# Performance work log

Hardware: AMD Instinct MI355X
Metric: run time of the kernel (lower is better)

The kernel has to match this reference:

```python
import jax, jax.numpy as jnp
import numpy as np

BUCKET_BINS = jnp.array([0, 1, 2, 3, 4, 5, 7, 8, 9, 10, 15, 16, 31, 32, 63, 64], dtype=jnp.int64)
POS_NUM = 28  # ZHPosTaging.pos_num; table size pos_num + 1


def setup_inputs() -> dict:
    key = jax.random.key(0)
    k1, k2, k3, k4, k5 = jax.random.split(key, 5)
    B, S, D = 4, 2048, 768
    N = 4096
    W, P = 20, 20
    x = jax.random.normal(k1, (B, S, D), dtype=jnp.float32)
    spans = jnp.sort(jax.random.randint(k2, (N, 2), 0, S, dtype=jnp.int64), axis=-1)
    pt_labels = jax.random.randint(k3, (S,), 0, POS_NUM + 1, dtype=jnp.int64)
    width_table = jax.random.normal(k4, (16, W), dtype=jnp.float32)
    pos_table = jax.random.normal(k5, (POS_NUM + 1, P), dtype=jnp.float32)
    return {"x": x, "spans": spans, "pt_labels": pt_labels,
            "width_table": width_table, "pos_table": pos_table}


def reference(x, spans, pt_labels, width_table, pos_table):
    # x: [B,S,D], spans: [N,2] with s0<=s1, pt_labels: [S]
    s0, s1 = spans[:, 0], spans[:, 1]                      # [N]
    width = s1 - s0 + 1                                    # [N], >= 1
    # bucket index: last ix with width >= BUCKET_BINS[ix]
    em = jnp.searchsorted(BUCKET_BINS, width, side='right') - 1
    width_emb = width_table[em]                            # [N,W]
    pos_emb0 = pos_table[pt_labels[s0]]                    # [N,P]
    pos_emb1 = pos_table[pt_labels[s1]]                    # [N,P]
    # segment mean over x[:, s0:s1+1] via exclusive cumsum
    cs = jnp.concatenate([jnp.zeros_like(x[:, :1]), jnp.cumsum(x, axis=1)], axis=1)  # [B,S+1,D]
    span_sum = cs[:, s1 + 1] - cs[:, s0]                   # [B,N,D]
    mean_vec = span_sum / width[None, :, None].astype(x.dtype)
    xs0 = x[:, s0]                                         # [B,N,D]
    xs1 = x[:, s1]                                         # [B,N,D]
    B, N = x.shape[0], spans.shape[0]
    bcast = lambda e: jnp.broadcast_to(e[None], (B, N, e.shape[-1]))
    return jnp.concatenate(
        [mean_vec, xs0, bcast(pos_emb0), xs1, bcast(pos_emb1), bcast(width_emb)],
        axis=-1)                                           # [B,N,3D+2P+W]
```

## Files before the change

kernel.cpp:

```cpp
#include <hip/hip_runtime.h>

#define BB   4
#define SS   2048
#define DD   768
#define NN   4096
#define PW   20
#define CH   16
#define NCH  128
#define ROW  2364

typedef float f4 __attribute__((ext_vector_type(4)));

__global__ __launch_bounds__(256) void partial_kernel(const float* __restrict__ x,
                                                      float* __restrict__ partial) {
    int d = blockIdx.x * 256 + threadIdx.x;
    int c = blockIdx.y;
    int b = blockIdx.z;
    const float* xp = x + ((size_t)(b * SS + c * CH)) * DD + d;
    float s = 0.f;
#pragma unroll
    for (int i = 0; i < CH; ++i) s += xp[(size_t)i * DD];
    partial[(b * NCH + c) * DD + d] = s;
}

__global__ __launch_bounds__(256) void prefix_kernel(float* __restrict__ partial) {
    int t = blockIdx.x * 256 + threadIdx.x;
    int b = t / DD;
    int d = t - b * DD;
    float* p = partial + (size_t)b * NCH * DD + d;
    float v[NCH];
#pragma unroll
    for (int c = 0; c < NCH; ++c) v[c] = p[(size_t)c * DD];
    float run = 0.f;
#pragma unroll
    for (int c = 0; c < NCH; ++c) { float nv = run + v[c]; p[(size_t)c * DD] = run; run = nv; }
}

__global__ __launch_bounds__(256) void cumsum_kernel(const float* __restrict__ x,
                                                     const float* __restrict__ partial,
                                                     float* __restrict__ cs) {
    int d = blockIdx.x * 256 + threadIdx.x;
    int c = blockIdx.y;
    int b = blockIdx.z;
    float run = partial[(b * NCH + c) * DD + d];
    const float* xp = x + ((size_t)(b * SS) + c * CH) * DD + d;
    float*       cp = cs + ((size_t)(b * (SS + 1)) + c * CH + 1) * DD + d;
    if (c == 0) cs[((size_t)(b * (SS + 1))) * DD + d] = 0.f;
    float v[CH];
#pragma unroll
    for (int i = 0; i < CH; ++i) v[i] = xp[(size_t)i * DD];
#pragma unroll
    for (int i = 0; i < CH; ++i) { run += v[i]; cp[(size_t)i * DD] = run; }
}

__global__ __launch_bounds__(192) void gather_kernel(const float* __restrict__ x,
                                                     const int* __restrict__ spans,
                                                     const int* __restrict__ pt_labels,
                                                     const float* __restrict__ wtab,
                                                     const float* __restrict__ ptab,
                                                     const float* __restrict__ cs,
                                                     float* __restrict__ out) {
    int n = blockIdx.x;
    int b = blockIdx.y;
    int t = threadIdx.x;

    int s0 = spans[2 * n];
    int s1 = spans[2 * n + 1];
    int width = s1 - s0 + 1;
    float inv_w = 1.0f / (float)width;

    const int bins[15] = {1, 2, 3, 4, 5, 7, 8, 9, 10, 15, 16, 31, 32, 63, 64};
    int em = 0;
#pragma unroll
    for (int i = 0; i < 15; ++i) em += (width >= bins[i]) ? 1 : 0;

    const f4* cs0 = (const f4*)(cs + ((size_t)(b * (SS + 1)) + s0) * DD);
    const f4* cs1 = (const f4*)(cs + ((size_t)(b * (SS + 1)) + s1 + 1) * DD);
    const f4* x0  = (const f4*)(x + ((size_t)(b * SS) + s0) * DD);
    const f4* x1  = (const f4*)(x + ((size_t)(b * SS) + s1) * DD);
    f4* o = (f4*)(out + ((size_t)(b * NN) + n) * ROW);

    f4 a  = cs0 == cs1 ? cs1[t] : cs1[t];
    f4 c0 = cs0[t];
    f4 v0 = x0[t];
    f4 v1 = x1[t];
    f4 m = (a - c0) * inv_w;
    __builtin_nontemporal_store(m,  o + t);
    __builtin_nontemporal_store(v0, o + 192 + t);
    __builtin_nontemporal_store(v1, o + 389 + t);

    if (t < 15) {
        int l0 = pt_labels[s0];
        int l1 = pt_labels[s1];
        if (t < 5) {
            f4 e = ((const f4*)(ptab + l0 * PW))[t];
            __builtin_nontemporal_store(e, o + 384 + t);
        } else if (t < 10) {
            f4 e = ((const f4*)(ptab + l1 * PW))[t - 5];
            __builtin_nontemporal_store(e, o + 581 + (t - 5));
        } else {
            f4 e = ((const f4*)(wtab + em * PW))[t - 10];
            __builtin_nontemporal_store(e, o + 586 + (t - 10));
        }
    }
}

extern "C" void kernel_launch(void* const* d_in, const int* in_sizes, int n_in,
                              void* d_out, int out_size, void* d_ws, size_t ws_size,
                              hipStream_t stream) {
    const float* x     = (const float*)d_in[0];
    const int*   spans = (const int*)d_in[1];
    const int*   pt    = (const int*)d_in[2];
    const float* wtab  = (const float*)d_in[3];
    const float* ptab  = (const float*)d_in[4];
    float* out = (float*)d_out;

    float* cs      = (float*)d_ws;
    float* partial = cs + (size_t)BB * (SS + 1) * DD;

    dim3 g1(3, NCH, BB);
    partial_kernel<<<g1, 256, 0, stream>>>(x, partial);
    prefix_kernel<<<12, 256, 0, stream>>>(partial);
    cumsum_kernel<<<g1, 256, 0, stream>>>(x, partial, cs);
    gather_kernel<<<dim3(NN, BB), 192, 0, stream>>>(x, spans, pt, wtab, ptab, cs, out);
}
```

Before: 213.6 us.

## Vectorize cumsum kernels with float4 and fold batch loop into gather blocks

```diff
diff --git a/kernel.cpp b/kernel.cpp
--- a/kernel.cpp
+++ b/kernel.cpp
@@ -8,19 +8,22 @@
 #define CH   16
 #define NCH  128
 #define ROW  2364
+#define DQ   192
 
 typedef float f4 __attribute__((ext_vector_type(4)));
 
 __global__ __launch_bounds__(256) void partial_kernel(const float* __restrict__ x,
                                                       float* __restrict__ partial) {
-    int d = blockIdx.x * 256 + threadIdx.x;
-    int c = blockIdx.y;
-    int b = blockIdx.z;
-    const float* xp = x + ((size_t)(b * SS + c * CH)) * DD + d;
-    float s = 0.f;
+    int tid = blockIdx.x * 256 + threadIdx.x;
+    int b = tid / (NCH * DQ);
+    int r = tid - b * (NCH * DQ);
+    int c = r / DQ;
+    int q = r - c * DQ;
+    const f4* xp = (const f4*)x + ((size_t)(b * SS + c * CH)) * DQ + q;
+    f4 s = {0.f, 0.f, 0.f, 0.f};
 #pragma unroll
-    for (int i = 0; i < CH; ++i) s += xp[(size_t)i * DD];
-    partial[(b * NCH + c) * DD + d] = s;
+    for (int i = 0; i < CH; ++i) s += xp[(size_t)i * DQ];
+    ((f4*)partial)[((size_t)(b * NCH + c)) * DQ + q] = s;
 }
 
 __global__ __launch_bounds__(256) void prefix_kernel(float* __restrict__ partial) {
@@ -39,18 +42,23 @@
 __global__ __launch_bounds__(256) void cumsum_kernel(const float* __restrict__ x,
                                                      const float* __restrict__ partial,
                                                      float* __restrict__ cs) {
-    int d = blockIdx.x * 256 + threadIdx.x;
-    int c = blockIdx.y;
-    int b = blockIdx.z;
-    float run = partial[(b * NCH + c) * DD + d];
-    const float* xp = x + ((size_t)(b * SS) + c * CH) * DD + d;
-    float*       cp = cs + ((size_t)(b * (SS + 1)) + c * CH + 1) * DD + d;
-    if (c == 0) cs[((size_t)(b * (SS + 1))) * DD + d] = 0.f;
-    float v[CH];
+    int tid = blockIdx.x * 256 + threadIdx.x;
+    int b = tid / (NCH * DQ);
+    int r = tid - b * (NCH * DQ);
+    int c = r / DQ;
+    int q = r - c * DQ;
+    f4 run = ((const f4*)partial)[((size_t)(b * NCH + c)) * DQ + q];
+    const f4* xp = (const f4*)x + ((size_t)(b * SS + c * CH)) * DQ + q;
+    f4*       cp = (f4*)cs + ((size_t)(b * (SS + 1) + c * CH + 1)) * DQ + q;
+    if (c == 0) {
+        f4 z = {0.f, 0.f, 0.f, 0.f};
+        ((f4*)cs)[((size_t)(b * (SS + 1))) * DQ + q] = z;
+    }
+    f4 v[CH];
 #pragma unroll
-    for (int i = 0; i < CH; ++i) v[i] = xp[(size_t)i * DD];
+    for (int i = 0; i < CH; ++i) v[i] = xp[(size_t)i * DQ];
 #pragma unroll
-    for (int i = 0; i < CH; ++i) { run += v[i]; cp[(size_t)i * DD] = run; }
+    for (int i = 0; i < CH; ++i) { run += v[i]; cp[(size_t)i * DQ] = run; }
 }
 
 __global__ __launch_bounds__(192) void gather_kernel(const float* __restrict__ x,
@@ -61,7 +69,6 @@
                                                      const float* __restrict__ cs,
                                                      float* __restrict__ out) {
     int n = blockIdx.x;
-    int b = blockIdx.y;
     int t = threadIdx.x;
 
     int s0 = spans[2 * n];
@@ -74,33 +81,46 @@
 #pragma unroll
     for (int i = 0; i < 15; ++i) em += (width >= bins[i]) ? 1 : 0;
 
-    const f4* cs0 = (const f4*)(cs + ((size_t)(b * (SS + 1)) + s0) * DD);
-    const f4* cs1 = (const f4*)(cs + ((size_t)(b * (SS + 1)) + s1 + 1) * DD);
-    const f4* x0  = (const f4*)(x + ((size_t)(b * SS) + s0) * DD);
-    const f4* x1  = (const f4*)(x + ((size_t)(b * SS) + s1) * DD);
-    f4* o = (f4*)(out + ((size_t)(b * NN) + n) * ROW);
-
-    f4 a  = cs0 == cs1 ? cs1[t] : cs1[t];
-    f4 c0 = cs0[t];
-    f4 v0 = x0[t];
-    f4 v1 = x1[t];
-    f4 m = (a - c0) * inv_w;
-    __builtin_nontemporal_store(m,  o + t);
-    __builtin_nontemporal_store(v0, o + 192 + t);
-    __builtin_nontemporal_store(v1, o + 389 + t);
+    f4 a[BB], c0[BB], v0[BB], v1[BB];
+#pragma unroll
+    for (int b = 0; b < BB; ++b) {
+        const f4* cs0 = (const f4*)cs + ((size_t)(b * (SS + 1) + s0)) * DQ;
+        const f4* cs1 = (const f4*)cs + ((size_t)(b * (SS + 1) + s1 + 1)) * DQ;
+        const f4* x0  = (const f4*)x  + ((size_t)(b * SS + s0)) * DQ;
+        const f4* x1  = (const f4*)x  + ((size_t)(b * SS + s1)) * DQ;
+        a[b]  = cs1[t];
+        c0[b] = cs0[t];
+        v0[b] = x0[t];
+        v1[b] = x1[t];
+    }
+#pragma unroll
+    for (int b = 0; b < BB; ++b) {
+        f4* o = (f4*)(out + ((size_t)(b * NN) + n) * ROW);
+        f4 m = (a[b] - c0[b]) * inv_w;
+        __builtin_nontemporal_store(m,     o + t);
+        __builtin_nontemporal_store(v0[b], o + 192 + t);
+        __builtin_nontemporal_store(v1[b], o + 389 + t);
+    }
 
     if (t < 15) {
-        int l0 = pt_labels[s0];
-        int l1 = pt_labels[s1];
+        f4 e;
+        int slot;
         if (t < 5) {
-            f4 e = ((const f4*)(ptab + l0 * PW))[t];
-            __builtin_nontemporal_store(e, o + 384 + t);
+            int l0 = pt_labels[s0];
+            e = ((const f4*)(ptab + l0 * PW))[t];
+            slot = 384 + t;
         } else if (t < 10) {
-            f4 e = ((const f4*)(ptab + l1 * PW))[t - 5];
-            __builtin_nontemporal_store(e, o + 581 + (t - 5));
+            int l1 = pt_labels[s1];
+            e = ((const f4*)(ptab + l1 * PW))[t - 5];
+            slot = 581 + (t - 5);
         } else {
-            f4 e = ((const f4*)(wtab + em * PW))[t - 10];
-            __builtin_nontemporal_store(e, o + 586 + (t - 10));
+            e = ((const f4*)(wtab + em * PW))[t - 10];
+            slot = 586 + (t - 10);
+        }
+#pragma unroll
+        for (int b = 0; b < BB; ++b) {
+            f4* o = (f4*)(out + ((size_t)(b * NN) + n) * ROW);
+            __builtin_nontemporal_store(e, o + slot);
         }
     }
 }
@@ -118,9 +138,9 @@
     float* cs      = (float*)d_ws;
     float* partial = cs + (size_t)BB * (SS + 1) * DD;
 
-    dim3 g1(3, NCH, BB);
-    partial_kernel<<<g1, 256, 0, stream>>>(x, partial);
+    const int NB = (BB * NCH * DQ) / 256;
+    partial_kernel<<<NB, 256, 0, stream>>>(x, partial);
     prefix_kernel<<<12, 256, 0, stream>>>(partial);
-    cumsum_kernel<<<g1, 256, 0, stream>>>(x, partial, cs);
-    gather_kernel<<<dim3(NN, BB), 192, 0, stream>>>(x, spans, pt, wtab, ptab, cs, out);
+    cumsum_kernel<<<NB, 256, 0, stream>>>(x, partial, cs);
+    gather_kernel<<<NN, 192, 0, stream>>>(x, spans, pt, wtab, ptab, cs, out);
 }
```

New measurement: 218.9 us. 2.5% more time.
